# Performance work log

Hardware: AMD Instinct MI355X
Metric: run time of the kernel (lower is better)

The kernel has to match this reference:

```python
import math
import jax, jax.numpy as jnp
import numpy as np

B, T, N, FIN, D, H, HM, L, P, O = 8, 12, 512, 3, 128, 4, 256, 3, 12, 1


def _pe(t, d):
    pos = jnp.arange(t, dtype=jnp.float32)[:, None]
    div = jnp.exp(jnp.arange(0, d, 2, dtype=jnp.float32) * (-math.log(10000.0) / d))
    pe = jnp.zeros((t, d), jnp.float32)
    pe = pe.at[:, 0::2].set(jnp.sin(pos * div))
    pe = pe.at[:, 1::2].set(jnp.cos(pos * div))
    return pe


def _spatial_attn(x, qkvW, qkvb, pW, pb):
    # attention over the node axis, per (batch, time)
    b, t, n, d = x.shape
    hd = d // H
    scale = hd ** -0.5
    qkv = jnp.einsum('btnd,ced->cbtne', x, qkvW) + qkvb[:, None, None, None, :]
    q, k, v = [a.reshape(b, t, n, H, hd) for a in qkv]
    a = jax.nn.softmax(jnp.einsum('btihe,btjhe->bthij', q, k) * scale, axis=-1)
    o = jnp.einsum('bthij,btjhe->btihe', a, v).reshape(b, t, n, d)
    return jnp.einsum('btnd,od->btno', o, pW) + pb


def _temporal_attn(x, qkvW, qkvb, pW, pb):
    # attention over the time axis, per (batch, node)
    b, t, n, d = x.shape
    hd = d // H
    scale = hd ** -0.5
    qkv = jnp.einsum('btnd,ced->cbtne', x, qkvW) + qkvb[:, None, None, None, :]
    q, k, v = [a.reshape(b, t, n, H, hd) for a in qkv]
    a = jax.nn.softmax(jnp.einsum('bxnhe,bynhe->bnhxy', q, k) * scale, axis=-1)
    o = jnp.einsum('bnhxy,bynhe->bxnhe', a, v).reshape(b, t, n, d)
    return jnp.einsum('btnd,od->btno', o, pW) + pb


def _layernorm(x, g, b, eps=1e-5):
    mu = x.mean(-1, keepdims=True)
    var = ((x - mu) ** 2).mean(-1, keepdims=True)
    return (x - mu) / jnp.sqrt(var + eps) * g + b


def setup_inputs() -> dict:
    key = jax.random.key(0)
    ks = iter(jax.random.split(key, 40))
    s = 0.02
    rn = lambda shape: jax.random.normal(next(ks), shape, jnp.float32) * s
    inp = {
        'x': jax.random.normal(next(ks), (B, T, N, FIN), jnp.float32),
        'tok_W': rn((D, FIN)), 'tok_b': rn((D,)),
        't_qkvW': rn((L, 3, D, D)), 't_qkvb': rn((L, 3, D)),
        't_pW': rn((L, D, D)), 't_pb': rn((L, D)),
        'g_qkvW': rn((L, 3, D, D)), 'g_qkvb': rn((L, 3, D)),
        'g_pW': rn((L, D, D)), 'g_pb': rn((L, D)),
        's_qkvW': rn((L, 3, D, D)), 's_qkvb': rn((L, 3, D)),
        's_pW': rn((L, D, D)), 's_pb': rn((L, D)),
        'resW': rn((L, D, D)), 'resb': rn((L, D)),
        'normW': jnp.ones((L, D), jnp.float32), 'normb': jnp.zeros((L, D), jnp.float32),
        'fc1W': rn((L, HM, 2 * D)), 'fc1b': rn((L, HM)),
        'fc2W': rn((L, D, HM)), 'fc2b': rn((L, D)),
        'end1W': rn((P, T)), 'end1b': rn((P,)),
        'end2W': rn((O, L * D)), 'end2b': rn((O,)),
    }
    return inp


def reference(x, tok_W, tok_b, t_qkvW, t_qkvb, t_pW, t_pb,
              g_qkvW, g_qkvb, g_pW, g_pb, s_qkvW, s_qkvb, s_pW, s_pb,
              resW, resb, normW, normb, fc1W, fc1b, fc2W, fc2b,
              end1W, end1b, end2W, end2b):
    # DataEmbedding: token linear + sinusoidal positional encoding over T
    h = jnp.einsum('btnf,df->btnd', x, tok_W) + tok_b
    h = h + _pe(h.shape[1], h.shape[3])[None, :, None, :]
    outs = []
    for l in range(t_qkvW.shape[0]):
        residual = h
        h = _temporal_attn(h, t_qkvW[l], t_qkvb[l], t_pW[l], t_pb[l])
        geo = _spatial_attn(h, g_qkvW[l], g_qkvb[l], g_pW[l], g_pb[l])
        sem = _spatial_attn(h, s_qkvW[l], s_qkvb[l], s_pW[l], s_pb[l])
        cat = jnp.concatenate([geo, sem], axis=-1)
        m = jax.nn.gelu(jnp.einsum('btnc,hc->btnh', cat, fc1W[l]) + fc1b[l], approximate=False)
        m = jnp.einsum('btnh,oh->btno', m, fc2W[l]) + fc2b[l]
        pre = jnp.einsum('btnd,od->btno', residual, resW[l]) + resb[l] + m
        h = _layernorm(pre, normW[l], normb[l])
        outs.append(h)
    xc = jnp.concatenate(outs, axis=-1)  # [B,T,N,L*D]
    y = jax.nn.relu(jnp.einsum('btnc,pt->bpnc', xc, end1W) + end1b[None, :, None, None])
    y = jnp.einsum('bpnc,oc->bpno', y, end2W) + end2b
    return y  # [B, pred_len, N, output_size]; structure_kl_loss is identically 0
```

## Files before the change

kernel.cpp:

```cpp
#include <hip/hip_runtime.h>
#include <hip/hip_bf16.h>
#include <math.h>

#define BB 8
#define TT 12
#define NN 512
#define FIN 3
#define DD 128
#define HH 4
#define HD 32
#define HMID 256
#define LL 3
#define PP 12
#define BTOK (TT*NN)

typedef short bf16x8 __attribute__((ext_vector_type(8)));
typedef float f32x4  __attribute__((ext_vector_type(4)));

__device__ __forceinline__ unsigned short f2bf(float f) {
    unsigned u = __float_as_uint(f);
    unsigned r = u + 0x7fffu + ((u >> 16) & 1u);
    return (unsigned short)(r >> 16);
}
__device__ __forceinline__ float bf2f(short s) {
    return __uint_as_float((unsigned)(unsigned short)s << 16);
}

__global__ __launch_bounds__(256)
void convert_weights_kernel(const float* __restrict__ t_qkvW, const float* __restrict__ t_pW,
                            const float* __restrict__ g_qkvW, const float* __restrict__ g_pW,
                            const float* __restrict__ s_qkvW, const float* __restrict__ s_pW,
                            const float* __restrict__ resW, const float* __restrict__ fc1W,
                            const float* __restrict__ fc2W, short* __restrict__ dst)
{
    int base = (blockIdx.x * 256 + threadIdx.x) * 4;
    const float* src; int off;
    if      (base < 147456) { src = t_qkvW; off = 0; }
    else if (base < 196608) { src = t_pW;   off = 147456; }
    else if (base < 344064) { src = g_qkvW; off = 196608; }
    else if (base < 393216) { src = g_pW;   off = 344064; }
    else if (base < 540672) { src = s_qkvW; off = 393216; }
    else if (base < 589824) { src = s_pW;   off = 540672; }
    else if (base < 638976) { src = resW;   off = 589824; }
    else if (base < 835584) { src = fc1W;   off = 638976; }
    else                    { src = fc2W;   off = 835584; }
    float4 v = *(const float4*)(src + (base - off));
    unsigned lo = f2bf(v.x) | ((unsigned)f2bf(v.y) << 16);
    unsigned hi = f2bf(v.z) | ((unsigned)f2bf(v.w) << 16);
    *(uint2*)(dst + base) = make_uint2(lo, hi);
}

__global__ __launch_bounds__(256)
void embed_kernel(const float* __restrict__ x, const float* __restrict__ tokW,
                  const float* __restrict__ tokb, short* __restrict__ h)
{
    int gid = blockIdx.x * 256 + threadIdx.x;
    int d = gid & (DD - 1);
    int token = gid >> 7;
    int t = (token / NN) % TT;
    const float* xp = x + (size_t)token * FIN;
    float v = tokb[d] + xp[0]*tokW[d*3+0] + xp[1]*tokW[d*3+1] + xp[2]*tokW[d*3+2];
    int de = d & ~1;
    float freq = __expf(-(float)de * (9.210340371976184f / (float)DD));
    float ang = (float)t * freq;
    v += (d & 1) ? cosf(ang) : sinf(ang);
    h[gid] = (short)f2bf(v);
}

template<int ACT, bool OBF16>
__device__ __forceinline__ void gemm_core(
    const short* __restrict__ Ap, int lda, const short* __restrict__ W, int K,
    const float* __restrict__ bias, const float* __restrict__ addsrc, int ald,
    void* __restrict__ outp, int ldc)
{
    __shared__ __align__(16) short As[64][72];
    __shared__ __align__(16) short Bs[128][72];
    const int tid = threadIdx.x;
    const int lane = tid & 63, w = tid >> 6;
    const int wm = (w & 1) * 32, wn = (w >> 1) * 64;
    const int l15 = lane & 15, lq = lane >> 4;
    f32x4 acc[2][4] = {};
    const int arow = tid >> 2, achk = (tid & 3) * 16;
    const int brow = tid >> 1, bchk = (tid & 1) * 32;

    for (int k0 = 0; k0 < K; k0 += 64) {
        const short* ap = Ap + (size_t)arow * lda + k0 + achk;
        *(uint4*)&As[arow][achk]     = *(const uint4*)ap;
        *(uint4*)&As[arow][achk + 8] = *(const uint4*)(ap + 8);
        const short* wp = W + (size_t)brow * K + k0 + bchk;
        #pragma unroll
        for (int i = 0; i < 4; ++i)
            *(uint4*)&Bs[brow][bchk + i*8] = *(const uint4*)(wp + i*8);
        __syncthreads();
        #pragma unroll
        for (int kc = 0; kc < 2; ++kc) {
            bf16x8 af[2], bfv[4];
            #pragma unroll
            for (int mi = 0; mi < 2; ++mi)
                af[mi] = *(const bf16x8*)&As[wm + mi*16 + l15][kc*32 + lq*8];
            #pragma unroll
            for (int nj = 0; nj < 4; ++nj)
                bfv[nj] = *(const bf16x8*)&Bs[wn + nj*16 + l15][kc*32 + lq*8];
            #pragma unroll
            for (int mi = 0; mi < 2; ++mi)
                #pragma unroll
                for (int nj = 0; nj < 4; ++nj)
                    acc[mi][nj] = __builtin_amdgcn_mfma_f32_16x16x32_bf16(
                        af[mi], bfv[nj], acc[mi][nj], 0, 0, 0);
        }
        __syncthreads();
    }

    #pragma unroll
    for (int nj = 0; nj < 4; ++nj) {
        int col = wn + nj * 16 + l15;
        float bv = bias[col];
        #pragma unroll
        for (int mi = 0; mi < 2; ++mi) {
            #pragma unroll
            for (int r = 0; r < 4; ++r) {
                int row = wm + mi * 16 + lq * 4 + r;
                float v = acc[mi][nj][r] + bv;
                if (addsrc) v += addsrc[(size_t)row * ald + col];
                if (ACT == 1) v = 0.5f * v * (1.0f + erff(v * 0.7071067811865476f));
                if (OBF16) ((short*)outp)[(size_t)row * ldc + col] = (short)f2bf(v);
                else       ((float*)outp)[(size_t)row * ldc + col] = v;
            }
        }
    }
}

template<int ACT, bool OBF16>
__global__ __launch_bounds__(256)
void gemm_plain(const short* __restrict__ A, const short* __restrict__ W,
                const float* __restrict__ bias, const float* __restrict__ addsrc,
                void* __restrict__ out, int K, int lda, int ldc, int ald)
{
    size_t bm = (size_t)blockIdx.x * 64;
    int bn = blockIdx.y * 128;
    void* op = OBF16 ? (void*)((short*)out + bm * ldc + bn)
                     : (void*)((float*)out + bm * ldc + bn);
    const float* ad = addsrc ? addsrc + bm * ald + bn : nullptr;
    gemm_core<ACT, OBF16>(A + bm * lda, lda, W + (size_t)bn * K, K, bias + bn,
                          ad, ald, op, ldc);
}

__global__ __launch_bounds__(256)
void gemm_qkv_gs(const short* __restrict__ A, const short* __restrict__ W1,
                 const short* __restrict__ W2, const float* __restrict__ b1,
                 const float* __restrict__ b2, short* __restrict__ out)
{
    size_t bm = (size_t)blockIdx.x * 64;
    int y = blockIdx.y;
    const short* W = (y < 3) ? W1 : W2;
    const float* b = (y < 3) ? b1 : b2;
    int wc = ((y < 3) ? y : y - 3) * 128;
    gemm_core<0, true>(A + bm * 128, 128, W + (size_t)wc * 128, 128,
                       b + wc, nullptr, 0, out + bm * 768 + y * 128, 768);
}

__global__ __launch_bounds__(256)
void gemm_proj_gs(const short* __restrict__ A, const short* __restrict__ W1,
                  const short* __restrict__ W2, const float* __restrict__ b1,
                  const float* __restrict__ b2, short* __restrict__ out)
{
    size_t bm = (size_t)blockIdx.x * 64;
    int sel = blockIdx.y;
    gemm_core<0, true>(A + bm * 256 + sel * 128, 256, sel ? W2 : W1, 128,
                       sel ? b2 : b1, nullptr, 0, out + bm * 256 + sel * 128, 256);
}

__global__ __launch_bounds__(192)
void temporal_attn_kernel(const short* __restrict__ qkv, short* __restrict__ out)
{
    __shared__ __align__(16) short kvs[4][TT][264];
    const int tid = threadIdx.x;
    const int bn0 = blockIdx.x * 4;

    #pragma unroll
    for (int i = 0; i < 8; ++i) {
        int flat = (i*192 + tid) * 8;
        int ns = flat / 3072;
        int rem = flat - ns*3072;
        int t = rem >> 8, c = rem & 255;
        int bn = bn0 + ns;
        int b = bn >> 9, n = bn & (NN - 1);
        const short* src = qkv + ((size_t)(b*TT + t) * NN + n) * 384 + 128 + c;
        *(uint4*)&kvs[ns][t][c] = *(const uint4*)src;
    }

    const int nsub = tid / 48;
    const int r = tid - nsub*48;
    const int h = r / TT, ti = r - h*TT;
    const int bn = bn0 + nsub;
    const int b = bn >> 9, n = bn & (NN - 1);
    const float qscale = 0.17677669529663687f * 1.4426950408889634f;

    float q[32];
    {
        const short* qp = qkv + ((size_t)(b*TT + ti) * NN + n) * 384 + h*HD;
        #pragma unroll
        for (int i = 0; i < 16; ++i) {
            unsigned u = ((const unsigned*)qp)[i];
            q[2*i]   = __uint_as_float(u << 16) * qscale;
            q[2*i+1] = __uint_as_float(u & 0xffff0000u) * qscale;
        }
    }
    __syncthreads();

    float s[TT];
    #pragma unroll
    for (int tj = 0; tj < TT; ++tj) {
        const unsigned* kr = (const unsigned*)&kvs[nsub][tj][h*HD];
        float d0 = 0.f, d1 = 0.f;
        #pragma unroll
        for (int i = 0; i < 16; ++i) {
            unsigned u = kr[i];
            d0 += q[2*i]   * __uint_as_float(u << 16);
            d1 += q[2*i+1] * __uint_as_float(u & 0xffff0000u);
        }
        s[tj] = d0 + d1;
    }
    float sum = 0.f, p[TT];
    #pragma unroll
    for (int tj = 0; tj < TT; ++tj) { p[tj] = __builtin_amdgcn_exp2f(s[tj]); sum += p[tj]; }
    float inv = 1.f / sum;

    float o[32];
    #pragma unroll
    for (int e = 0; e < 32; ++e) o[e] = 0.f;
    #pragma unroll
    for (int tj = 0; tj < TT; ++tj) {
        const unsigned* vr = (const unsigned*)&kvs[nsub][tj][128 + h*HD];
        float pj = p[tj];
        #pragma unroll
        for (int i = 0; i < 16; ++i) {
            unsigned u = vr[i];
            o[2*i]   += pj * __uint_as_float(u << 16);
            o[2*i+1] += pj * __uint_as_float(u & 0xffff0000u);
        }
    }

    short* op = out + ((size_t)(b*TT + ti) * NN + n) * DD + h*HD;
    #pragma unroll
    for (int i = 0; i < 16; ++i) {
        unsigned pk = f2bf(o[2*i] * inv) | ((unsigned)f2bf(o[2*i+1] * inv) << 16);
        ((unsigned*)op)[i] = pk;
    }
}

__global__ __launch_bounds__(256)
void spatial_attn_mfma_kernel(const short* __restrict__ qkv, short* __restrict__ out)
{
    __shared__ __align__(16) short Qs[128][40];
    __shared__ __align__(16) short Ks[64][40];
    __shared__ __align__(16) short Vt[36][72];
    __shared__ __align__(16) short Ps[4][32][72];

    const int tid = threadIdx.x;
    const int bid = blockIdx.x;
    const int sel = bid & 1;
    const int qb = (bid >> 1) & 3;
    const int h = (bid >> 3) & 3;
    const int bt = bid >> 5;
    const int lane = tid & 63, w = tid >> 6;
    const int l15 = lane & 15, lq = lane >> 4;

    const size_t btbase = (size_t)bt * NN * 768 + sel * 384 + h * HD;
    const float qscale = 0.17677669529663687f * 1.4426950408889634f;

    {
        int r = tid >> 1, hf = (tid & 1) * 16;
        const short* qp = qkv + btbase + (size_t)(qb*128 + r) * 768 + hf;
        short tmp[16];
        #pragma unroll
        for (int i = 0; i < 16; ++i) tmp[i] = (short)f2bf(bf2f(qp[i]) * qscale);
        *(uint4*)&Qs[r][hf]     = *(const uint4*)tmp;
        *(uint4*)&Qs[r][hf + 8] = *(const uint4*)(tmp + 8);
    }
    for (int idx = tid; idx < 4*72; idx += 256) {
        int rr = idx / 72, cc = idx - rr*72;
        Vt[32 + rr][cc] = (rr == 0 && cc < 64) ? (short)0x3F80 : (short)0;
    }

    f32x4 acc_o[2][3] = {};
    const int ve = tid & 31, vkb = (tid >> 5) * 8;

    for (int kt = 0; kt < 8; ++kt) {
        __syncthreads();
        {
            int r = tid >> 2, c = (tid & 3) * 8;
            const short* kp = qkv + btbase + (size_t)(kt*64 + r) * 768 + 128 + c;
            *(uint4*)&Ks[r][c] = *(const uint4*)kp;
        }
        {
            const short* vp = qkv + btbase + (size_t)(kt*64 + vkb) * 768 + 256 + ve;
            short tmp[8];
            #pragma unroll
            for (int jj = 0; jj < 8; ++jj) tmp[jj] = vp[(size_t)jj * 768];
            *(uint4*)&Vt[ve][vkb] = *(const uint4*)tmp;
        }
        __syncthreads();

        bf16x8 kf[4], qf[2];
        #pragma unroll
        for (int km = 0; km < 4; ++km)
            kf[km] = *(const bf16x8*)&Ks[km*16 + l15][lq*8];
        #pragma unroll
        for (int qn = 0; qn < 2; ++qn)
            qf[qn] = *(const bf16x8*)&Qs[w*32 + qn*16 + l15][lq*8];
        f32x4 sacc[4][2] = {};
        #pragma unroll
        for (int km = 0; km < 4; ++km)
            #pragma unroll
            for (int qn = 0; qn < 2; ++qn)
                sacc[km][qn] = __builtin_amdgcn_mfma_f32_16x16x32_bf16(
                    kf[km], qf[qn], sacc[km][qn], 0, 0, 0);

        #pragma unroll
        for (int km = 0; km < 4; ++km)
            #pragma unroll
            for (int qn = 0; qn < 2; ++qn) {
                float e0 = __builtin_amdgcn_exp2f(sacc[km][qn][0]);
                float e1 = __builtin_amdgcn_exp2f(sacc[km][qn][1]);
                float e2 = __builtin_amdgcn_exp2f(sacc[km][qn][2]);
                float e3 = __builtin_amdgcn_exp2f(sacc[km][qn][3]);
                unsigned lo = f2bf(e0) | ((unsigned)f2bf(e1) << 16);
                unsigned hi = f2bf(e2) | ((unsigned)f2bf(e3) << 16);
                *(uint2*)&Ps[w][qn*16 + l15][km*16 + lq*4] = make_uint2(lo, hi);
            }

        #pragma unroll
        for (int kk = 0; kk < 2; ++kk) {
            bf16x8 pa[2], vb[3];
            #pragma unroll
            for (int mi = 0; mi < 2; ++mi)
                pa[mi] = *(const bf16x8*)&Ps[w][mi*16 + l15][kk*32 + lq*8];
            #pragma unroll
            for (int nj = 0; nj < 3; ++nj)
                vb[nj] = *(const bf16x8*)&Vt[nj*16 + l15][kk*32 + lq*8];
            #pragma unroll
            for (int mi = 0; mi < 2; ++mi)
                #pragma unroll
                for (int nj = 0; nj < 3; ++nj)
                    acc_o[mi][nj] = __builtin_amdgcn_mfma_f32_16x16x32_bf16(
                        pa[mi], vb[nj], acc_o[mi][nj], 0, 0, 0);
        }
    }

    #pragma unroll
    for (int mi = 0; mi < 2; ++mi) {
        #pragma unroll
        for (int r = 0; r < 4; ++r) {
            float l = __shfl(acc_o[mi][2][r], lane & 48);
            float inv = 1.f / l;
            int qrow = qb*128 + w*32 + mi*16 + lq*4 + r;
            short* op = out + ((size_t)bt * NN + qrow) * 256 + sel*128 + h*HD;
            op[l15]      = (short)f2bf(acc_o[mi][0][r] * inv);
            op[16 + l15] = (short)f2bf(acc_o[mi][1][r] * inv);
        }
    }
}

__global__ __launch_bounds__(256)
void layernorm_kernel(const float* __restrict__ in, const float* __restrict__ g,
                      const float* __restrict__ bta, short* __restrict__ outh,
                      float* __restrict__ xc, int lcol)
{
    int tid = threadIdx.x;
    int wave = tid >> 6, lane = tid & 63;
    size_t token = (size_t)blockIdx.x * 4 + wave;
    const float* row = in + token * DD;
    float x0 = row[lane], x1 = row[lane + 64];
    float s = x0 + x1, ss = x0*x0 + x1*x1;
    #pragma unroll
    for (int off = 1; off < 64; off <<= 1) {
        s  += __shfl_xor(s,  off);
        ss += __shfl_xor(ss, off);
    }
    float mu = s * (1.f / DD);
    float var = ss * (1.f / DD) - mu * mu;
    float rstd = rsqrtf(var + 1e-5f);
    float y0 = (x0 - mu) * rstd * g[lane]      + bta[lane];
    float y1 = (x1 - mu) * rstd * g[lane + 64] + bta[lane + 64];
    outh[token*DD + lane]      = (short)f2bf(y0);
    outh[token*DD + lane + 64] = (short)f2bf(y1);
    xc[token*(LL*DD) + lcol + lane]      = y0;
    xc[token*(LL*DD) + lcol + lane + 64] = y1;
}

__global__ __launch_bounds__(256)
void head_kernel(const float* __restrict__ xc, const float* __restrict__ e1W,
                 const float* __restrict__ e1b, const float* __restrict__ e2W,
                 const float* __restrict__ e2b, float* __restrict__ out)
{
    __shared__ float xcs[TT][LL*DD];
    __shared__ float w1[PP*TT];
    int bid = blockIdx.x;
    int b = bid >> 9, n = bid & (NN - 1);
    int tid = threadIdx.x;
    if (tid < PP*TT) w1[tid] = e1W[tid];
    #pragma unroll
    for (int i = 0; i < 18; ++i) {
        int f = i*256 + tid;
        int t = f / (LL*DD), c = f % (LL*DD);
        xcs[t][c] = xc[(((size_t)(b*TT + t) * NN) + n) * (LL*DD) + c];
    }
    __syncthreads();
    int p = tid >> 4, lane16 = tid & 15;
    float acc = 0.f;
    if (p < PP) {
        for (int c = lane16; c < LL*DD; c += 16) {
            float tmp = e1b[p];
            #pragma unroll
            for (int t = 0; t < TT; ++t) tmp += xcs[t][c] * w1[p*TT + t];
            tmp = fmaxf(tmp, 0.f);
            acc += tmp * e2W[c];
        }
    }
    acc += __shfl_xor(acc, 1);
    acc += __shfl_xor(acc, 2);
    acc += __shfl_xor(acc, 4);
    acc += __shfl_xor(acc, 8);
    if (p < PP && lane16 == 0)
        out[((size_t)(b*PP + p)) * NN + n] = acc + e2b[0];
}

extern "C" void kernel_launch(void* const* d_in, const int* in_sizes, int n_in,
                              void* d_out, int out_size, void* d_ws, size_t ws_size,
                              hipStream_t stream)
{
    const float* x      = (const float*)d_in[0];
    const float* tok_W  = (const float*)d_in[1];
    const float* tok_b  = (const float*)d_in[2];
    const float* t_qkvW = (const float*)d_in[3];
    const float* t_qkvb = (const float*)d_in[4];
    const float* t_pW   = (const float*)d_in[5];
    const float* t_pb   = (const float*)d_in[6];
    const float* g_qkvW = (const float*)d_in[7];
    const float* g_qkvb = (const float*)d_in[8];
    const float* g_pW   = (const float*)d_in[9];
    const float* g_pb   = (const float*)d_in[10];
    const float* s_qkvW = (const float*)d_in[11];
    const float* s_qkvb = (const float*)d_in[12];
    const float* s_pW   = (const float*)d_in[13];
    const float* s_pb   = (const float*)d_in[14];
    const float* resW   = (const float*)d_in[15];
    const float* resb   = (const float*)d_in[16];
    const float* normW  = (const float*)d_in[17];
    const float* normb  = (const float*)d_in[18];
    const float* fc1W   = (const float*)d_in[19];
    const float* fc1b   = (const float*)d_in[20];
    const float* fc2W   = (const float*)d_in[21];
    const float* fc2b   = (const float*)d_in[22];
    const float* end1W  = (const float*)d_in[23];
    const float* end1b  = (const float*)d_in[24];
    const float* end2W  = (const float*)d_in[25];
    const float* end2b  = (const float*)d_in[26];
    float* out = (float*)d_out;

    short* wbf = (short*)d_ws;
    const size_t WBF = 933888;
    convert_weights_kernel<<<912, 256, 0, stream>>>(
        t_qkvW, t_pW, g_qkvW, g_pW, s_qkvW, s_pW, resW, fc1W, fc2W, wbf);

    const size_t perBatchBytes = (size_t)BTOK * 2304 * 2;
    int nb = 8;
    while (nb > 1 && WBF*2 + (size_t)nb * perBatchBytes > ws_size) nb >>= 1;

    for (int b0 = 0; b0 < BB; b0 += nb) {
        const int CT = nb * BTOK;
        const int GM = CT / 64;
        short* act  = wbf + WBF;
        short* h    = act;
        short* ht   = h    + (size_t)CT*128;
        short* qkvh = ht   + (size_t)CT*128;
        short* m1   = qkvh;
        float* m2   = (float*)(qkvh + (size_t)CT*256);
        float* pre  = m2 + (size_t)CT*128;
        short* atmp = qkvh + (size_t)CT*768;
        short* cat  = atmp + (size_t)CT*256;
        float* xc   = (float*)(cat + (size_t)CT*256);

        const float* xch = x + (size_t)b0 * BTOK * FIN;
        float* outch = out + (size_t)b0 * PP * NN;

        embed_kernel<<<CT*DD/256, 256, 0, stream>>>(xch, tok_W, tok_b, h);

        for (int l = 0; l < LL; ++l) {
            const short* tqw = wbf + 0      + (size_t)l*49152;
            const short* tpw = wbf + 147456 + (size_t)l*16384;
            const short* gqw = wbf + 196608 + (size_t)l*49152;
            const short* gpw = wbf + 344064 + (size_t)l*16384;
            const short* sqw = wbf + 393216 + (size_t)l*49152;
            const short* spw = wbf + 540672 + (size_t)l*16384;
            const short* rsw = wbf + 589824 + (size_t)l*16384;
            const short* f1w = wbf + 638976 + (size_t)l*65536;
            const short* f2w = wbf + 835584 + (size_t)l*32768;
            const float* tqb = t_qkvb + (size_t)l*384;
            const float* tpb = t_pb   + (size_t)l*128;
            const float* gqb = g_qkvb + (size_t)l*384;
            const float* gpb = g_pb   + (size_t)l*128;
            const float* sqb = s_qkvb + (size_t)l*384;
            const float* spb = s_pb   + (size_t)l*128;

            gemm_plain<0,true><<<dim3(GM,3), 256, 0, stream>>>(
                h, tqw, tqb, nullptr, qkvh, 128, 128, 384, 0);
            temporal_attn_kernel<<<nb*NN/4, 192, 0, stream>>>(qkvh, atmp);
            gemm_plain<0,true><<<dim3(GM,1), 256, 0, stream>>>(
                atmp, tpw, tpb, nullptr, ht, 128, 128, 128, 0);

            gemm_qkv_gs<<<dim3(GM,6), 256, 0, stream>>>(ht, gqw, sqw, gqb, sqb, qkvh);
            spatial_attn_mfma_kernel<<<nb*TT*HH*4*2, 256, 0, stream>>>(qkvh, atmp);
            gemm_proj_gs<<<dim3(GM,2), 256, 0, stream>>>(atmp, gpw, spw, gpb, spb, cat);

            gemm_plain<1,true><<<dim3(GM,2), 256, 0, stream>>>(
                cat, f1w, fc1b + (size_t)l*HMID, nullptr, m1, 256, 256, 256, 0);
            gemm_plain<0,false><<<dim3(GM,1), 256, 0, stream>>>(
                m1, f2w, fc2b + (size_t)l*128, nullptr, m2, 256, 256, 128, 0);
            gemm_plain<0,false><<<dim3(GM,1), 256, 0, stream>>>(
                h, rsw, resb + (size_t)l*128, m2, pre, 128, 128, 128, 128);
            layernorm_kernel<<<CT/4, 256, 0, stream>>>(pre, normW + (size_t)l*128,
                                                       normb + (size_t)l*128, h, xc, l*DD);
        }

        head_kernel<<<nb*NN, 256, 0, stream>>>(xc, end1W, end1b, end2W, end2b, outch);
    }
}
```

Measured before the change: 795.7 us.

## Fold attention output projections into following linear weights

A new setup kernel precomputes, per layer, the product of each spatial QKV weight with the temporal output projection, and the product of fc1 with the geo and semantic output projections. Biases are folded the same way. This removes three projection GEMM launches per layer and the intermediate ht and cat buffers. Float-to-bf16 packing now uses the hardware paired conversion intrinsic. The combined weights are rounded to bf16 after the fp32 product, which changes numerics slightly, and the setup kernel runs on every call.

```diff
diff --git a/kernel.cpp b/kernel.cpp
--- a/kernel.cpp
+++ b/kernel.cpp
@@ -24,6 +24,10 @@
 }
 __device__ __forceinline__ float bf2f(short s) {
     return __uint_as_float((unsigned)(unsigned short)s << 16);
+}
+__device__ __forceinline__ unsigned pk2bf(float a, float b) {
+    __hip_bfloat162 h = __float22bfloat162_rn(make_float2(a, b));
+    return *(unsigned*)&h;
 }
 
 __global__ __launch_bounds__(256)
@@ -45,9 +49,86 @@
     else if (base < 835584) { src = fc1W;   off = 638976; }
     else                    { src = fc2W;   off = 835584; }
     float4 v = *(const float4*)(src + (base - off));
-    unsigned lo = f2bf(v.x) | ((unsigned)f2bf(v.y) << 16);
-    unsigned hi = f2bf(v.z) | ((unsigned)f2bf(v.w) << 16);
-    *(uint2*)(dst + base) = make_uint2(lo, hi);
+    *(uint2*)(dst + base) = make_uint2(pk2bf(v.x, v.y), pk2bf(v.z, v.w));
+}
+
+__global__ __launch_bounds__(256)
+void combine_weights_kernel(const float* __restrict__ g_qkvW, const float* __restrict__ s_qkvW,
+                            const float* __restrict__ t_pW, const float* __restrict__ g_pW,
+                            const float* __restrict__ s_pW, const float* __restrict__ g_qkvb,
+                            const float* __restrict__ s_qkvb, const float* __restrict__ t_pb,
+                            const float* __restrict__ g_pb, const float* __restrict__ s_pb,
+                            const float* __restrict__ fc1W, const float* __restrict__ fc1b,
+                            short* __restrict__ wbf, float* __restrict__ qkvb2,
+                            float* __restrict__ fc1b2)
+{
+    __shared__ float Bs[128][128];
+    const int tid = threadIdx.x;
+    const int blk = blockIdx.x;
+    const float* A; const float* B; int arst;
+    short* outp; int orst;
+    int l, sel, c = 0, half = 0;
+    const bool isqkv = blk < 18;
+    if (isqkv) {
+        l = blk / 6; int r = blk % 6; sel = r / 3; c = r % 3;
+        A = (sel ? s_qkvW : g_qkvW) + (size_t)(l*3 + c) * 16384;  arst = 128;
+        B = t_pW + (size_t)l * 16384;
+        outp = wbf + (sel ? 393216 : 196608) + (size_t)l*49152 + (size_t)c*16384;
+        orst = 128;
+    } else {
+        int r = blk - 18; l = r / 4; r %= 4; sel = r >> 1; half = r & 1;
+        A = fc1W + (size_t)(l*256 + half*128) * 256 + sel*128;    arst = 256;
+        B = (sel ? s_pW : g_pW) + (size_t)l * 16384;
+        outp = wbf + 638976 + (size_t)l*65536 + (size_t)half*32768 + sel*128;
+        orst = 256;
+    }
+    for (int idx = tid; idx < 16384; idx += 256)
+        Bs[idx >> 7][idx & 127] = B[idx];
+    __syncthreads();
+
+    const int e = tid >> 1, db = (tid & 1) * 64;
+    const float* Arow = A + (size_t)e * arst;
+    #pragma unroll 1
+    for (int ch = 0; ch < 4; ++ch) {
+        float acc[16] = {};
+        for (int o4 = 0; o4 < 32; ++o4) {
+            float4 a4 = *(const float4*)(Arow + o4*4);
+            float as[4] = {a4.x, a4.y, a4.z, a4.w};
+            #pragma unroll
+            for (int k = 0; k < 4; ++k) {
+                #pragma unroll
+                for (int j4 = 0; j4 < 4; ++j4) {
+                    float4 b = *(const float4*)&Bs[o4*4 + k][db + ch*16 + j4*4];
+                    acc[j4*4+0] += as[k]*b.x;
+                    acc[j4*4+1] += as[k]*b.y;
+                    acc[j4*4+2] += as[k]*b.z;
+                    acc[j4*4+3] += as[k]*b.w;
+                }
+            }
+        }
+        short* orow = outp + (size_t)e * orst + db + ch*16;
+        #pragma unroll
+        for (int j = 0; j < 8; ++j)
+            ((unsigned*)orow)[j] = pk2bf(acc[2*j], acc[2*j+1]);
+    }
+
+    if (tid < 128) {
+        if (isqkv) {
+            const float* tb = t_pb + l*128;
+            const float* ar = A + (size_t)tid * 128;
+            float s = (sel ? s_qkvb : g_qkvb)[(l*3 + c)*128 + tid];
+            for (int o = 0; o < 128; ++o) s += ar[o] * tb[o];
+            qkvb2[l*768 + sel*384 + c*128 + tid] = s;
+        } else if (sel == 0) {
+            int hg = half*128 + tid;
+            const float* frow = fc1W + (size_t)(l*256 + hg) * 256;
+            const float* gb = g_pb + l*128;
+            const float* sb = s_pb + l*128;
+            float s = fc1b[l*256 + hg];
+            for (int o = 0; o < 128; ++o) s += frow[o]*gb[o] + frow[128+o]*sb[o];
+            fc1b2[l*256 + hg] = s;
+        }
+    }
 }
 
 __global__ __launch_bounds__(256)
@@ -159,17 +240,6 @@
                        b + wc, nullptr, 0, out + bm * 768 + y * 128, 768);
 }
 
-__global__ __launch_bounds__(256)
-void gemm_proj_gs(const short* __restrict__ A, const short* __restrict__ W1,
-                  const short* __restrict__ W2, const float* __restrict__ b1,
-                  const float* __restrict__ b2, short* __restrict__ out)
-{
-    size_t bm = (size_t)blockIdx.x * 64;
-    int sel = blockIdx.y;
-    gemm_core<0, true>(A + bm * 256 + sel * 128, 256, sel ? W2 : W1, 128,
-                       sel ? b2 : b1, nullptr, 0, out + bm * 256 + sel * 128, 256);
-}
-
 __global__ __launch_bounds__(192)
 void temporal_attn_kernel(const short* __restrict__ qkv, short* __restrict__ out)
 {
@@ -243,10 +313,8 @@
 
     short* op = out + ((size_t)(b*TT + ti) * NN + n) * DD + h*HD;
     #pragma unroll
-    for (int i = 0; i < 16; ++i) {
-        unsigned pk = f2bf(o[2*i] * inv) | ((unsigned)f2bf(o[2*i+1] * inv) << 16);
-        ((unsigned*)op)[i] = pk;
-    }
+    for (int i = 0; i < 16; ++i)
+        ((unsigned*)op)[i] = pk2bf(o[2*i] * inv, o[2*i+1] * inv);
 }
 
 __global__ __launch_bounds__(256)
@@ -271,12 +339,16 @@
 
     {
         int r = tid >> 1, hf = (tid & 1) * 16;
-        const short* qp = qkv + btbase + (size_t)(qb*128 + r) * 768 + hf;
-        short tmp[16];
-        #pragma unroll
-        for (int i = 0; i < 16; ++i) tmp[i] = (short)f2bf(bf2f(qp[i]) * qscale);
+        const unsigned* qp = (const unsigned*)(qkv + btbase + (size_t)(qb*128 + r) * 768 + hf);
+        unsigned tmp[8];
+        #pragma unroll
+        for (int i = 0; i < 8; ++i) {
+            unsigned u = qp[i];
+            tmp[i] = pk2bf(__uint_as_float(u << 16) * qscale,
+                           __uint_as_float(u & 0xffff0000u) * qscale);
+        }
         *(uint4*)&Qs[r][hf]     = *(const uint4*)tmp;
-        *(uint4*)&Qs[r][hf + 8] = *(const uint4*)(tmp + 8);
+        *(uint4*)&Qs[r][hf + 8] = *(const uint4*)(tmp + 4);
     }
     for (int idx = tid; idx < 4*72; idx += 256) {
         int rr = idx / 72, cc = idx - rr*72;
@@ -325,9 +397,8 @@
                 float e1 = __builtin_amdgcn_exp2f(sacc[km][qn][1]);
                 float e2 = __builtin_amdgcn_exp2f(sacc[km][qn][2]);
                 float e3 = __builtin_amdgcn_exp2f(sacc[km][qn][3]);
-                unsigned lo = f2bf(e0) | ((unsigned)f2bf(e1) << 16);
-                unsigned hi = f2bf(e2) | ((unsigned)f2bf(e3) << 16);
-                *(uint2*)&Ps[w][qn*16 + l15][km*16 + lq*4] = make_uint2(lo, hi);
+                *(uint2*)&Ps[w][qn*16 + l15][km*16 + lq*4] =
+                    make_uint2(pk2bf(e0, e1), pk2bf(e2, e3));
             }
 
         #pragma unroll
@@ -461,26 +532,31 @@
 
     short* wbf = (short*)d_ws;
     const size_t WBF = 933888;
+    float* qkvb2 = (float*)(wbf + WBF);
+    float* fc1b2 = qkvb2 + 2304;
+    short* act   = (short*)(fc1b2 + 768);
+
     convert_weights_kernel<<<912, 256, 0, stream>>>(
         t_qkvW, t_pW, g_qkvW, g_pW, s_qkvW, s_pW, resW, fc1W, fc2W, wbf);
-
-    const size_t perBatchBytes = (size_t)BTOK * 2304 * 2;
+    combine_weights_kernel<<<30, 256, 0, stream>>>(
+        g_qkvW, s_qkvW, t_pW, g_pW, s_pW, g_qkvb, s_qkvb, t_pb, g_pb, s_pb,
+        fc1W, fc1b, wbf, qkvb2, fc1b2);
+
+    const size_t fixedBytes = WBF*2 + 3072*4;
+    const size_t perBatchBytes = (size_t)BTOK * 2432 * 2;
     int nb = 8;
-    while (nb > 1 && WBF*2 + (size_t)nb * perBatchBytes > ws_size) nb >>= 1;
+    while (nb > 1 && fixedBytes + (size_t)nb * perBatchBytes > ws_size) nb >>= 1;
 
     for (int b0 = 0; b0 < BB; b0 += nb) {
         const int CT = nb * BTOK;
         const int GM = CT / 64;
-        short* act  = wbf + WBF;
         short* h    = act;
-        short* ht   = h    + (size_t)CT*128;
-        short* qkvh = ht   + (size_t)CT*128;
+        short* qkvh = h + (size_t)CT*128;
         short* m1   = qkvh;
-        float* m2   = (float*)(qkvh + (size_t)CT*256);
+        short* atmp = qkvh + (size_t)CT*768;
+        float* m2   = (float*)(atmp + (size_t)CT*256);
         float* pre  = m2 + (size_t)CT*128;
-        short* atmp = qkvh + (size_t)CT*768;
-        short* cat  = atmp + (size_t)CT*256;
-        float* xc   = (float*)(cat + (size_t)CT*256);
+        float* xc   = pre + (size_t)CT*128;
 
         const float* xch = x + (size_t)b0 * BTOK * FIN;
         float* outch = out + (size_t)b0 * PP * NN;
@@ -489,33 +565,23 @@
 
         for (int l = 0; l < LL; ++l) {
             const short* tqw = wbf + 0      + (size_t)l*49152;
-            const short* tpw = wbf + 147456 + (size_t)l*16384;
             const short* gqw = wbf + 196608 + (size_t)l*49152;
-            const short* gpw = wbf + 344064 + (size_t)l*16384;
             const short* sqw = wbf + 393216 + (size_t)l*49152;
-            const short* spw = wbf + 540672 + (size_t)l*16384;
             const short* rsw = wbf + 589824 + (size_t)l*16384;
             const short* f1w = wbf + 638976 + (size_t)l*65536;
             const short* f2w = wbf + 835584 + (size_t)l*32768;
             const float* tqb = t_qkvb + (size_t)l*384;
-            const float* tpb = t_pb   + (size_t)l*128;
-            const float* gqb = g_qkvb + (size_t)l*384;
-            const float* gpb = g_pb   + (size_t)l*128;
-            const float* sqb = s_qkvb + (size_t)l*384;
-            const float* spb = s_pb   + (size_t)l*128;
 
             gemm_plain<0,true><<<dim3(GM,3), 256, 0, stream>>>(
                 h, tqw, tqb, nullptr, qkvh, 128, 128, 384, 0);
             temporal_attn_kernel<<<nb*NN/4, 192, 0, stream>>>(qkvh, atmp);
-            gemm_plain<0,true><<<dim3(GM,1), 256, 0, stream>>>(
-                atmp, tpw, tpb, nullptr, ht, 128, 128, 128, 0);
-
-            gemm_qkv_gs<<<dim3(GM,6), 256, 0, stream>>>(ht, gqw, sqw, gqb, sqb, qkvh);
+
+            gemm_qkv_gs<<<dim3(GM,6), 256, 0, stream>>>(
+                atmp, gqw, sqw, qkvb2 + l*768, qkvb2 + l*768 + 384, qkvh);
             spatial_attn_mfma_kernel<<<nb*TT*HH*4*2, 256, 0, stream>>>(qkvh, atmp);
-            gemm_proj_gs<<<dim3(GM,2), 256, 0, stream>>>(atmp, gpw, spw, gpb, spb, cat);
 
             gemm_plain<1,true><<<dim3(GM,2), 256, 0, stream>>>(
-                cat, f1w, fc1b + (size_t)l*HMID, nullptr, m1, 256, 256, 256, 0);
+                atmp, f1w, fc1b2 + l*256, nullptr, m1, 256, 256, 256, 0);
             gemm_plain<0,false><<<dim3(GM,1), 256, 0, stream>>>(
                 m1, f2w, fc2b + (size_t)l*128, nullptr, m2, 256, 256, 128, 0);
             gemm_plain<0,false><<<dim3(GM,1), 256, 0, stream>>>(
```

Measured after the change: 769.5 us. -3.3%, faster.
